# Optimization experiments

Measured on AMD Instinct MI355X. Metric: run time of the kernel, lower is better.

Reference implementation:

```python
import jax, jax.numpy as jnp
import numpy as np

FP16_MAX = 65504.0  # clamp_fp16 bound
GROUP = 64          # SVDQuant int4 group size along in_features


def _int4_quant_dequant(w):
    """Symmetric per-(out_channel, group) int4 fake-quant of a weight [out, in].
    Emulates the W4 weight numerics of SVDQW4A4Linear at the dequantized level."""
    o, i = w.shape
    wg = w.reshape(o, i // GROUP, GROUP)
    scale = np.max(np.abs(wg), axis=-1, keepdims=True) / 7.0
    scale = np.where(scale == 0.0, 1.0, scale)
    q = np.clip(np.round(wg / scale), -8, 7)
    return (q * scale).reshape(o, i).astype(np.float32)


def setup_inputs() -> dict:
    dim, hidden = 3072, 8192
    B, S = 2, 4096
    rng = np.random.default_rng(0)
    # fused [w1; w3] weight: [2*hidden, dim]; down proj w2: [dim, hidden]
    w13 = _int4_quant_dequant((rng.standard_normal((2 * hidden, dim)) * 0.02).astype(np.float32))
    w2 = _int4_quant_dequant((rng.standard_normal((dim, hidden)) * 0.02).astype(np.float32))
    key = jax.random.key(0)
    x = jax.random.normal(key, (B, S, dim), dtype=jnp.float32)
    return {"x": x, "w13": jnp.asarray(w13), "w2": jnp.asarray(w2)}


def reference(x, w13, w2):
    # fused gate/up projection: [B,S,dim] @ [2H,dim]^T -> [B,S,2H]
    h = jnp.einsum("bsd,hd->bsh", x, w13)
    # NOTE: original code does `x3, x1 = x.chunk(2, dim=-1)` -> first half is x3
    x3, x1 = jnp.split(h, 2, axis=-1)
    g = jnp.clip(jax.nn.silu(x1) * x3, -FP16_MAX, FP16_MAX)  # clamp_fp16
    # down projection: [B,S,H] @ [dim,H]^T -> [B,S,dim]
    return jnp.einsum("bsh,dh->bsd", g, w2)
```

## Files before the change

kernel.cpp:

```cpp
#include <hip/hip_runtime.h>
#include <hip/hip_bf16.h>


typedef __attribute__((ext_vector_type(8))) __bf16 bf16x8;
typedef __attribute__((ext_vector_type(4))) float f32x4;

#define GLD_LDS16(gptr, lptr)                                                        \
  __builtin_amdgcn_global_load_lds(                                                  \
      (const __attribute__((address_space(1))) void*)(gptr),                         \
      (__attribute__((address_space(3))) void*)(lptr), 16, 0, 0)

#define VMCNT(n) asm volatile("s_waitcnt vmcnt(" #n ")" ::: "memory")
#define BAR()    __builtin_amdgcn_s_barrier()

#define MFMA16(a, b, c) __builtin_amdgcn_mfma_f32_16x16x32_bf16((a), (b), (c), 0, 0, 0)

__device__ __forceinline__ __bf16 bfr(float f) {
  unsigned int u = __builtin_bit_cast(unsigned int, f);
  unsigned short r = (unsigned short)((u + 0x7FFFu + ((u >> 16) & 1u)) >> 16);
  return __builtin_bit_cast(__bf16, r);
}

__global__ __launch_bounds__(256)
void k_cvt(const float* __restrict__ src, unsigned short* __restrict__ dst, long n) {
  long i = ((long)blockIdx.x * 256 + threadIdx.x) * 8;
  const long stride = (long)gridDim.x * 256 * 8;
  for (; i < n; i += stride) {
    float4 f0 = *(const float4*)(src + i);
    float4 f1 = *(const float4*)(src + i + 4);
    bf16x8 o;
    o[0] = bfr(f0.x); o[1] = bfr(f0.y); o[2] = bfr(f0.z); o[3] = bfr(f0.w);
    o[4] = bfr(f1.x); o[5] = bfr(f1.y); o[6] = bfr(f1.z); o[7] = bfr(f1.w);
    *(bf16x8*)(dst + i) = o;
  }
}

__global__ __launch_bounds__(512, 2)
void k_gateup11(const unsigned short* __restrict__ X,
                const unsigned short* __restrict__ W13,
                __hip_bfloat16* __restrict__ G)
{
  constexpr int K = 3072, LDG = 8192, NT = K / 64;
  __shared__ unsigned short lds[65536];

  const int t = threadIdx.x, l = t & 63, wid = t >> 6;
  const int wm = wid >> 2, wn = wid & 3;
  const int l15 = l & 15, lhi = l >> 4, sw = l15 & 7;

  const int bid = blockIdx.x;
  const int swz = (bid & 7) * 256 + (bid >> 3);
  const int mb = swz >> 6, nb = swz & 63;

  const int srow = t >> 3;
  const int scol = ((t & 7) ^ (srow & 7)) * 8;
  const unsigned short* xa = X   + (size_t)(mb * 256 + srow) * K + scol;
  const unsigned short* b3 = W13 + (size_t)(nb * 128 + srow) * K + scol;
  const unsigned short* b1 = W13 + (size_t)(8192 + nb * 128 + srow) * K + scol;
  const int lo = t * 8;

#define ST_A02(d, kt) do {                                                     \
    GLD_LDS16(xa + (kt),                 lds + (d) * 16384 + lo);              \
    GLD_LDS16(xa + (size_t)128 * K + (kt), lds + (d) * 16384 + 8192 + lo);     \
  } while (0)
#define ST_A13(d, kt) do {                                                     \
    GLD_LDS16(xa + (size_t)64 * K + (kt),  lds + (d) * 16384 + 4096 + lo);     \
    GLD_LDS16(xa + (size_t)192 * K + (kt), lds + (d) * 16384 + 12288 + lo);    \
  } while (0)
#define ST_B3(d, kt) do {                                                      \
    GLD_LDS16(b3 + (kt),                lds + 32768 + (d) * 8192 + lo);        \
    GLD_LDS16(b3 + (size_t)64 * K + (kt), lds + 32768 + (d) * 8192 + 4096 + lo); \
  } while (0)
#define ST_B1(d, kt) do {                                                      \
    GLD_LDS16(b1 + (kt),                lds + 49152 + (d) * 8192 + lo);        \
    GLD_LDS16(b1 + (size_t)64 * K + (kt), lds + 49152 + (d) * 8192 + 4096 + lo); \
  } while (0)

  f32x4 acc3[8][2], acc1[8][2];
#pragma unroll
  for (int m = 0; m < 8; ++m)
#pragma unroll
    for (int n = 0; n < 2; ++n) {
      acc3[m][n] = (f32x4){0.f, 0.f, 0.f, 0.f};
      acc1[m][n] = (f32x4){0.f, 0.f, 0.f, 0.f};
    }

  ST_B3(0, 0); ST_A02(0, 0); ST_B1(0, 0); ST_A13(0, 0);
  ST_B3(1, 64); ST_A02(1, 64); ST_B1(1, 64);
  VMCNT(6);
  BAR();

  for (int c = 0; c < NT; ++c) {
    const int d = c & 1, dn = d ^ 1;
    const int k1 = (c + 1 < NT ? c + 1 : 0) * 64;
    const int k2 = (c + 2 < NT ? c + 2 : 0) * 64;
    const int Ab = d * 16384, B3b = 32768 + d * 8192, B1b = 49152 + d * 8192;

    bf16x8 ra[4][2], rb[4][2], r3[2][2], r1[2][2];

#pragma unroll
    for (int mf = 0; mf < 4; ++mf)
#pragma unroll
      for (int kk = 0; kk < 2; ++kk)
        ra[mf][kk] = *(const bf16x8*)(lds + Ab + (wm * 128 + mf * 16 + l15) * 64 + ((kk * 4 + lhi) ^ sw) * 8);
#pragma unroll
    for (int nf = 0; nf < 2; ++nf)
#pragma unroll
      for (int kk = 0; kk < 2; ++kk)
        r3[nf][kk] = *(const bf16x8*)(lds + B3b + (wn * 32 + nf * 16 + l15) * 64 + ((kk * 4 + lhi) ^ sw) * 8);
    ST_A13(dn, k1);
    BAR();
    __builtin_amdgcn_s_setprio(1);
#pragma unroll
    for (int mf = 0; mf < 4; ++mf)
#pragma unroll
      for (int nf = 0; nf < 2; ++nf)
#pragma unroll
        for (int kk = 0; kk < 2; ++kk)
          acc3[mf][nf] = MFMA16(ra[mf][kk], r3[nf][kk], acc3[mf][nf]);
    __builtin_amdgcn_s_setprio(0);
    BAR();

#pragma unroll
    for (int nf = 0; nf < 2; ++nf)
#pragma unroll
      for (int kk = 0; kk < 2; ++kk)
        r1[nf][kk] = *(const bf16x8*)(lds + B1b + (wn * 32 + nf * 16 + l15) * 64 + ((kk * 4 + lhi) ^ sw) * 8);
    ST_B3(d, k2);
    BAR();
    __builtin_amdgcn_s_setprio(1);
#pragma unroll
    for (int mf = 0; mf < 4; ++mf)
#pragma unroll
      for (int nf = 0; nf < 2; ++nf)
#pragma unroll
        for (int kk = 0; kk < 2; ++kk)
          acc1[mf][nf] = MFMA16(ra[mf][kk], r1[nf][kk], acc1[mf][nf]);
    __builtin_amdgcn_s_setprio(0);
    BAR();

#pragma unroll
    for (int mf = 0; mf < 4; ++mf)
#pragma unroll
      for (int kk = 0; kk < 2; ++kk)
        rb[mf][kk] = *(const bf16x8*)(lds + Ab + (wm * 128 + 64 + mf * 16 + l15) * 64 + ((kk * 4 + lhi) ^ sw) * 8);
    ST_A02(d, k2);
    BAR();
    __builtin_amdgcn_s_setprio(1);
#pragma unroll
    for (int mf = 0; mf < 4; ++mf)
#pragma unroll
      for (int nf = 0; nf < 2; ++nf)
#pragma unroll
        for (int kk = 0; kk < 2; ++kk)
          acc3[4 + mf][nf] = MFMA16(rb[mf][kk], r3[nf][kk], acc3[4 + mf][nf]);
    __builtin_amdgcn_s_setprio(0);
    BAR();

    ST_B1(d, k2);
    VMCNT(6);
    BAR();
    __builtin_amdgcn_s_setprio(1);
#pragma unroll
    for (int mf = 0; mf < 4; ++mf)
#pragma unroll
      for (int nf = 0; nf < 2; ++nf)
#pragma unroll
        for (int kk = 0; kk < 2; ++kk)
          acc1[4 + mf][nf] = MFMA16(rb[mf][kk], r1[nf][kk], acc1[4 + mf][nf]);
    __builtin_amdgcn_s_setprio(0);
    BAR();
  }

  const int gr0 = mb * 256 + wm * 128;
  const int gc0 = nb * 128 + wn * 32;
#pragma unroll
  for (int mf = 0; mf < 8; ++mf) {
    const int ro = (mf >> 2) * 64 + (mf & 3) * 16;
#pragma unroll
    for (int nf = 0; nf < 2; ++nf)
#pragma unroll
      for (int r = 0; r < 4; ++r) {
        float h3 = acc3[mf][nf][r];
        float h1 = acc1[mf][nf][r];
        float s  = h1 / (1.f + __expf(-h1));
        float g  = fminf(fmaxf(s * h3, -65504.f), 65504.f);
        G[(size_t)(gr0 + ro + lhi * 4 + r) * LDG + (gc0 + nf * 16 + l15)] =
            __float2bfloat16(g);
      }
  }
#undef ST_A02
#undef ST_A13
#undef ST_B3
#undef ST_B1
}

__global__ __launch_bounds__(512, 2)
void k_down11(const unsigned short* __restrict__ Gm,
              const unsigned short* __restrict__ W2,
              float* __restrict__ Out)
{
  constexpr int K = 8192, LDO = 3072, NT = K / 64;
  __shared__ unsigned short lds[73728];

  const int t = threadIdx.x, l = t & 63, wid = t >> 6;
  const int wm = wid >> 1, wn = wid & 1;
  const int l15 = l & 15, lhi = l >> 4, sw = l15 & 7;

  const int bid = blockIdx.x;
  const int swz = (bid & 7) * 96 + (bid >> 3);
  const int mb = swz / 24, nb = swz % 24;

  const int srow = t >> 3;
  const int scol = ((t & 7) ^ (srow & 7)) * 8;
  const unsigned short* ga = Gm + (size_t)(mb * 256 + srow) * K + scol;
  const unsigned short* wb = W2 + (size_t)(nb * 128 + srow) * K + scol;
  const int lo = t * 8;

#define DST_A(e, kt) do {                                                       \
    GLD_LDS16(ga + (kt),                 lds + (e) * 16384 + lo);               \
    GLD_LDS16(ga + (size_t)64 * K + (kt),  lds + (e) * 16384 + 4096 + lo);      \
    GLD_LDS16(ga + (size_t)128 * K + (kt), lds + (e) * 16384 + 8192 + lo);      \
    GLD_LDS16(ga + (size_t)192 * K + (kt), lds + (e) * 16384 + 12288 + lo);     \
  } while (0)
#define DST_B(e, kt) do {                                                       \
    GLD_LDS16(wb + (kt),                lds + 49152 + (e) * 8192 + lo);         \
    GLD_LDS16(wb + (size_t)64 * K + (kt), lds + 49152 + (e) * 8192 + 4096 + lo); \
  } while (0)

  f32x4 acc[4][4];
#pragma unroll
  for (int mf = 0; mf < 4; ++mf)
#pragma unroll
    for (int nf = 0; nf < 4; ++nf)
      acc[mf][nf] = (f32x4){0.f, 0.f, 0.f, 0.f};

  DST_B(0, 0);  DST_A(0, 0);
  DST_B(1, 64); DST_A(1, 64);

  for (int c = 0; c < NT; ++c) {
    const int e = c % 3;
    const int eS = (c + 2) % 3;
    const int k2 = (c + 2 < NT ? c + 2 : 0) * 64;

    VMCNT(6);
    BAR();

    bf16x8 ra[4][2], rb[4][2];
#pragma unroll
    for (int mf = 0; mf < 4; ++mf)
#pragma unroll
      for (int kk = 0; kk < 2; ++kk)
        ra[mf][kk] = *(const bf16x8*)(lds + e * 16384 + (wm * 64 + mf * 16 + l15) * 64 + ((kk * 4 + lhi) ^ sw) * 8);
#pragma unroll
    for (int nf = 0; nf < 4; ++nf)
#pragma unroll
      for (int kk = 0; kk < 2; ++kk)
        rb[nf][kk] = *(const bf16x8*)(lds + 49152 + e * 8192 + (wn * 64 + nf * 16 + l15) * 64 + ((kk * 4 + lhi) ^ sw) * 8);

    DST_B(eS, k2);
    DST_A(eS, k2);

    __builtin_amdgcn_s_setprio(1);
#pragma unroll
    for (int mf = 0; mf < 4; ++mf)
#pragma unroll
      for (int nf = 0; nf < 4; ++nf)
#pragma unroll
        for (int kk = 0; kk < 2; ++kk)
          acc[mf][nf] = MFMA16(ra[mf][kk], rb[nf][kk], acc[mf][nf]);
    __builtin_amdgcn_s_setprio(0);
  }

  const int r0 = mb * 256 + wm * 64;
  const int c0 = nb * 128 + wn * 64;
#pragma unroll
  for (int mf = 0; mf < 4; ++mf)
#pragma unroll
    for (int nf = 0; nf < 4; ++nf)
#pragma unroll
      for (int r = 0; r < 4; ++r)
        Out[(size_t)(r0 + mf * 16 + lhi * 4 + r) * LDO + (c0 + nf * 16 + l15)] =
            acc[mf][nf][r];
#undef DST_A
#undef DST_B
}

extern "C" void kernel_launch(void* const* d_in, const int* in_sizes, int n_in,
                              void* d_out, int out_size, void* d_ws, size_t ws_size,
                              hipStream_t stream) {
  const float* x   = (const float*)d_in[0];
  const float* w13 = (const float*)d_in[1];
  const float* w2  = (const float*)d_in[2];
  float* out = (float*)d_out;

  const long NX = 25165824L, NW13 = 50331648L, NW2 = 25165824L;
  const size_t XB = 50331648, W13B = 100663296, W2B = 50331648;

  unsigned short* xb   = (unsigned short*)d_ws;
  unsigned short* w13b = (unsigned short*)((char*)d_ws + XB);
  unsigned short* w2b  = (unsigned short*)((char*)d_ws + XB + W13B);
  __hip_bfloat16* g    = (__hip_bfloat16*)((char*)d_ws + XB + W13B + W2B);

  k_cvt<<<2048, 256, 0, stream>>>(x,   xb,   NX);
  k_cvt<<<2048, 256, 0, stream>>>(w13, w13b, NW13);
  k_cvt<<<2048, 256, 0, stream>>>(w2,  w2b,  NW2);
  k_gateup11<<<2048, 512, 0, stream>>>(xb, w13b, g);
  k_down11<<<768, 512, 0, stream>>>((const unsigned short*)g, w2b, out);
}
```

Before: 1.195 ms.

## Restructure gate/up GEMM pipeline into two-phase double-buffer with fewer barriers

Replaces the four-phase, two-stage-ahead prefetch schedule in the gate/up kernel with a simpler double-buffered loop. It loads the whole 256-row A tile and both B halves for the next k-step while computing the current one. Each iteration now has two barriers instead of eight, and all eight A fragments are kept in registers at once. The aim is less synchronisation overhead, at the cost of higher register pressure and only a one-step prefetch distance, which may expose more memory latency.

```diff
diff --git a/kernel.cpp b/kernel.cpp
--- a/kernel.cpp
+++ b/kernel.cpp
@@ -36,7 +36,7 @@
 }
 
 __global__ __launch_bounds__(512, 2)
-void k_gateup11(const unsigned short* __restrict__ X,
+void k_gateup13(const unsigned short* __restrict__ X,
                 const unsigned short* __restrict__ W13,
                 __hip_bfloat16* __restrict__ G)
 {
@@ -58,21 +58,19 @@
   const unsigned short* b1 = W13 + (size_t)(8192 + nb * 128 + srow) * K + scol;
   const int lo = t * 8;
 
-#define ST_A02(d, kt) do {                                                     \
-    GLD_LDS16(xa + (kt),                 lds + (d) * 16384 + lo);              \
-    GLD_LDS16(xa + (size_t)128 * K + (kt), lds + (d) * 16384 + 8192 + lo);     \
-  } while (0)
-#define ST_A13(d, kt) do {                                                     \
-    GLD_LDS16(xa + (size_t)64 * K + (kt),  lds + (d) * 16384 + 4096 + lo);     \
-    GLD_LDS16(xa + (size_t)192 * K + (kt), lds + (d) * 16384 + 12288 + lo);    \
-  } while (0)
-#define ST_B3(d, kt) do {                                                      \
-    GLD_LDS16(b3 + (kt),                lds + 32768 + (d) * 8192 + lo);        \
-    GLD_LDS16(b3 + (size_t)64 * K + (kt), lds + 32768 + (d) * 8192 + 4096 + lo); \
-  } while (0)
-#define ST_B1(d, kt) do {                                                      \
-    GLD_LDS16(b1 + (kt),                lds + 49152 + (d) * 8192 + lo);        \
-    GLD_LDS16(b1 + (size_t)64 * K + (kt), lds + 49152 + (d) * 8192 + 4096 + lo); \
+#define STG_A(d, kt) do {                                                      \
+    GLD_LDS16(xa + (kt),                  lds + (d) * 32768 + lo);             \
+    GLD_LDS16(xa + (size_t)64 * K + (kt),  lds + (d) * 32768 + 4096 + lo);     \
+    GLD_LDS16(xa + (size_t)128 * K + (kt), lds + (d) * 32768 + 8192 + lo);     \
+    GLD_LDS16(xa + (size_t)192 * K + (kt), lds + (d) * 32768 + 12288 + lo);    \
+  } while (0)
+#define STG_B3(d, kt) do {                                                     \
+    GLD_LDS16(b3 + (kt),                 lds + (d) * 32768 + 16384 + lo);      \
+    GLD_LDS16(b3 + (size_t)64 * K + (kt), lds + (d) * 32768 + 20480 + lo);     \
+  } while (0)
+#define STG_B1(d, kt) do {                                                     \
+    GLD_LDS16(b1 + (kt),                 lds + (d) * 32768 + 24576 + lo);      \
+    GLD_LDS16(b1 + (size_t)64 * K + (kt), lds + (d) * 32768 + 28672 + lo);     \
   } while (0)
 
   f32x4 acc3[8][2], acc1[8][2];
@@ -84,98 +82,67 @@
       acc1[m][n] = (f32x4){0.f, 0.f, 0.f, 0.f};
     }
 
-  ST_B3(0, 0); ST_A02(0, 0); ST_B1(0, 0); ST_A13(0, 0);
-  ST_B3(1, 64); ST_A02(1, 64); ST_B1(1, 64);
-  VMCNT(6);
-  BAR();
+  STG_A(0, 0); STG_B3(0, 0); STG_B1(0, 0);
 
   for (int c = 0; c < NT; ++c) {
-    const int d = c & 1, dn = d ^ 1;
-    const int k1 = (c + 1 < NT ? c + 1 : 0) * 64;
-    const int k2 = (c + 2 < NT ? c + 2 : 0) * 64;
-    const int Ab = d * 16384, B3b = 32768 + d * 8192, B1b = 49152 + d * 8192;
-
-    bf16x8 ra[4][2], rb[4][2], r3[2][2], r1[2][2];
-
-#pragma unroll
-    for (int mf = 0; mf < 4; ++mf)
-#pragma unroll
-      for (int kk = 0; kk < 2; ++kk)
-        ra[mf][kk] = *(const bf16x8*)(lds + Ab + (wm * 128 + mf * 16 + l15) * 64 + ((kk * 4 + lhi) ^ sw) * 8);
+    const int R = c & 1, S = R ^ 1;
+    const int kn = (c + 1 < NT ? c + 1 : 0) * 64;
+    const int Ab = R * 32768, B3b = Ab + 16384, B1b = Ab + 24576;
+
+    VMCNT(2);
+    BAR();
+    bf16x8 ra[8][2], r3[2][2];
+#pragma unroll
+    for (int mf = 0; mf < 8; ++mf)
+#pragma unroll
+      for (int kk = 0; kk < 2; ++kk) {
+        const int row = wm * 128 + mf * 16 + l15;
+        ra[mf][kk] = *(const bf16x8*)(lds + Ab + row * 64 + ((kk * 4 + lhi) ^ sw) * 8);
+      }
 #pragma unroll
     for (int nf = 0; nf < 2; ++nf)
 #pragma unroll
-      for (int kk = 0; kk < 2; ++kk)
-        r3[nf][kk] = *(const bf16x8*)(lds + B3b + (wn * 32 + nf * 16 + l15) * 64 + ((kk * 4 + lhi) ^ sw) * 8);
-    ST_A13(dn, k1);
-    BAR();
+      for (int kk = 0; kk < 2; ++kk) {
+        const int row = wn * 32 + nf * 16 + l15;
+        r3[nf][kk] = *(const bf16x8*)(lds + B3b + row * 64 + ((kk * 4 + lhi) ^ sw) * 8);
+      }
+    STG_A(S, kn); STG_B3(S, kn);
     __builtin_amdgcn_s_setprio(1);
 #pragma unroll
-    for (int mf = 0; mf < 4; ++mf)
+    for (int mf = 0; mf < 8; ++mf)
 #pragma unroll
       for (int nf = 0; nf < 2; ++nf)
 #pragma unroll
         for (int kk = 0; kk < 2; ++kk)
           acc3[mf][nf] = MFMA16(ra[mf][kk], r3[nf][kk], acc3[mf][nf]);
     __builtin_amdgcn_s_setprio(0);
+
+    VMCNT(6);
     BAR();
-
+    bf16x8 r1[2][2];
 #pragma unroll
     for (int nf = 0; nf < 2; ++nf)
 #pragma unroll
-      for (int kk = 0; kk < 2; ++kk)
-        r1[nf][kk] = *(const bf16x8*)(lds + B1b + (wn * 32 + nf * 16 + l15) * 64 + ((kk * 4 + lhi) ^ sw) * 8);
-    ST_B3(d, k2);
-    BAR();
+      for (int kk = 0; kk < 2; ++kk) {
+        const int row = wn * 32 + nf * 16 + l15;
+        r1[nf][kk] = *(const bf16x8*)(lds + B1b + row * 64 + ((kk * 4 + lhi) ^ sw) * 8);
+      }
+    STG_B1(S, kn);
     __builtin_amdgcn_s_setprio(1);
 #pragma unroll
-    for (int mf = 0; mf < 4; ++mf)
+    for (int mf = 0; mf < 8; ++mf)
 #pragma unroll
       for (int nf = 0; nf < 2; ++nf)
 #pragma unroll
         for (int kk = 0; kk < 2; ++kk)
           acc1[mf][nf] = MFMA16(ra[mf][kk], r1[nf][kk], acc1[mf][nf]);
     __builtin_amdgcn_s_setprio(0);
-    BAR();
-
-#pragma unroll
-    for (int mf = 0; mf < 4; ++mf)
-#pragma unroll
-      for (int kk = 0; kk < 2; ++kk)
-        rb[mf][kk] = *(const bf16x8*)(lds + Ab + (wm * 128 + 64 + mf * 16 + l15) * 64 + ((kk * 4 + lhi) ^ sw) * 8);
-    ST_A02(d, k2);
-    BAR();
-    __builtin_amdgcn_s_setprio(1);
-#pragma unroll
-    for (int mf = 0; mf < 4; ++mf)
-#pragma unroll
-      for (int nf = 0; nf < 2; ++nf)
-#pragma unroll
-        for (int kk = 0; kk < 2; ++kk)
-          acc3[4 + mf][nf] = MFMA16(rb[mf][kk], r3[nf][kk], acc3[4 + mf][nf]);
-    __builtin_amdgcn_s_setprio(0);
-    BAR();
-
-    ST_B1(d, k2);
-    VMCNT(6);
-    BAR();
-    __builtin_amdgcn_s_setprio(1);
-#pragma unroll
-    for (int mf = 0; mf < 4; ++mf)
-#pragma unroll
-      for (int nf = 0; nf < 2; ++nf)
-#pragma unroll
-        for (int kk = 0; kk < 2; ++kk)
-          acc1[4 + mf][nf] = MFMA16(rb[mf][kk], r1[nf][kk], acc1[4 + mf][nf]);
-    __builtin_amdgcn_s_setprio(0);
-    BAR();
   }
 
   const int gr0 = mb * 256 + wm * 128;
   const int gc0 = nb * 128 + wn * 32;
 #pragma unroll
-  for (int mf = 0; mf < 8; ++mf) {
-    const int ro = (mf >> 2) * 64 + (mf & 3) * 16;
+  for (int mf = 0; mf < 8; ++mf)
 #pragma unroll
     for (int nf = 0; nf < 2; ++nf)
 #pragma unroll
@@ -184,14 +151,12 @@
         float h1 = acc1[mf][nf][r];
         float s  = h1 / (1.f + __expf(-h1));
         float g  = fminf(fmaxf(s * h3, -65504.f), 65504.f);
-        G[(size_t)(gr0 + ro + lhi * 4 + r) * LDG + (gc0 + nf * 16 + l15)] =
+        G[(size_t)(gr0 + mf * 16 + lhi * 4 + r) * LDG + (gc0 + nf * 16 + l15)] =
             __float2bfloat16(g);
       }
-  }
-#undef ST_A02
-#undef ST_A13
-#undef ST_B3
-#undef ST_B1
+#undef STG_A
+#undef STG_B3
+#undef STG_B1
 }
 
 __global__ __launch_bounds__(512, 2)
@@ -304,6 +269,6 @@
   k_cvt<<<2048, 256, 0, stream>>>(x,   xb,   NX);
   k_cvt<<<2048, 256, 0, stream>>>(w13, w13b, NW13);
   k_cvt<<<2048, 256, 0, stream>>>(w2,  w2b,  NW2);
-  k_gateup11<<<2048, 512, 0, stream>>>(xb, w13b, g);
+  k_gateup13<<<2048, 512, 0, stream>>>(xb, w13b, g);
   k_down11<<<768, 512, 0, stream>>>((const unsigned short*)g, w2b, out);
 }
```

After: 1.145 ms. -4.1%, faster.
